# Optimization experiments

Hardware: AMD Instinct MI355X
Metric: run time of the kernel (lower is better)

Reference implementation:

```python
import jax, jax.numpy as jnp
import numpy as np

H = 1024
BATCH, T = 16, 2048

def setup_inputs() -> dict:
    key = jax.random.key(0)
    k1, k2, k3, k4 = jax.random.split(key, 4)
    scale = 1.0 / (H ** 0.5)
    return {
        "u_sequence": jax.random.normal(k1, (BATCH, T, 1), dtype=jnp.float32),
        "A": jax.random.normal(k2, (H, H), dtype=jnp.float32) * scale,
        "B": jax.random.normal(k3, (H, 1), dtype=jnp.float32) * scale,
        "C": jax.random.normal(k4, (1, H), dtype=jnp.float32) * scale,
        "D": jnp.zeros((1,), dtype=jnp.float32),
    }

def reference(u_sequence, A, B, C, D):
    # u_sequence: [Bt, T, 1]
    u = u_sequence[..., 0]            # [Bt, T]
    b_vec = B[:, 0]                   # [H]

    def step(h, u_t):
        # h: [Bt, H], u_t: [Bt]
        h_new = h @ A.T + u_t[:, None] * b_vec[None, :]
        return h_new, h_new

    h0 = jnp.zeros((u.shape[0], H), dtype=u.dtype)
    _, h_stack = jax.lax.scan(step, h0, u.T)   # h_stack: [T, Bt, H]
    h_stack = jnp.swapaxes(h_stack, 0, 1)      # [Bt, T, H]
    y = jnp.einsum("bth,h->bt", h_stack, C[0]) + u * D[0]
    return y[..., None]                         # [Bt, T, 1]
```

## Files before the change

### kernel.cpp

```cpp
#include <hip/hip_runtime.h>

#define HDIM 1024
#define TLEN 2048
#define NBATCH 16

typedef short bf16x8 __attribute__((ext_vector_type(8)));
typedef float floatx4 __attribute__((ext_vector_type(4)));
typedef unsigned short ushort_t;

__device__ __forceinline__ ushort_t f2bf(float x) {
  unsigned u = __float_as_uint(x);
  unsigned r = (u + 0x7FFFu + ((u >> 16) & 1u)) >> 16;
  return (ushort_t)r;
}
__device__ __forceinline__ float bf2f(ushort_t h) {
  return __uint_as_float(((unsigned)h) << 16);
}

typedef __attribute__((address_space(1))) void gvoid_t;
typedef __attribute__((address_space(3))) void lvoid_t;
__device__ __forceinline__ void gload16(const ushort_t* g, ushort_t* l) {
  __builtin_amdgcn_global_load_lds((gvoid_t*)g, (lvoid_t*)l, 16, 0, 0);
}

#define TSTR 71

__global__ __launch_bounds__(256) void prep(const float* __restrict__ A,
    const float* __restrict__ Bv, const float* __restrict__ Cv,
    ushort_t* __restrict__ Ah, ushort_t* __restrict__ Am, ushort_t* __restrict__ Al,
    ushort_t* __restrict__ ATh, ushort_t* __restrict__ ATm, ushort_t* __restrict__ ATl,
    float* __restrict__ Vc, float* __restrict__ U) {
  __shared__ ushort_t Lt[3 * 64 * TSTR];
  const int tid = threadIdx.x;
  if (blockIdx.x >= 256) {
    int i = (blockIdx.x - 256) * 256 + tid;
    if (i < HDIM) Vc[i] = Bv[i];
    else U[i - HDIM] = Cv[i - HDIM];
    return;
  }
  const int row0 = (blockIdx.x >> 4) * 64, col0 = (blockIdx.x & 15) * 64;
  const int r = tid >> 2, q = tid & 3;
  ushort_t hs[16], ms[16], ls[16];
#pragma unroll
  for (int c4 = 0; c4 < 4; ++c4) {
    float4 a = *(const float4*)&A[(row0 + r) * HDIM + col0 + q * 16 + c4 * 4];
    float av[4] = {a.x, a.y, a.z, a.w};
#pragma unroll
    for (int i = 0; i < 4; ++i) {
      float z = av[i];
      ushort_t h = f2bf(z); float r1 = z - bf2f(h);
      ushort_t mq = f2bf(r1); float r2 = r1 - bf2f(mq);
      ushort_t lq = f2bf(r2);
      hs[c4 * 4 + i] = h; ms[c4 * 4 + i] = mq; ls[c4 * 4 + i] = lq;
    }
  }
  size_t go = (size_t)(row0 + r) * HDIM + col0 + q * 16;
  *(uint4*)&Ah[go] = ((uint4*)hs)[0]; *(uint4*)&Ah[go + 8] = ((uint4*)hs)[1];
  *(uint4*)&Am[go] = ((uint4*)ms)[0]; *(uint4*)&Am[go + 8] = ((uint4*)ms)[1];
  *(uint4*)&Al[go] = ((uint4*)ls)[0]; *(uint4*)&Al[go + 8] = ((uint4*)ls)[1];
#pragma unroll
  for (int i = 0; i < 16; ++i) {
    int c = q * 16 + i;
    Lt[0 * 64 * TSTR + r * TSTR + c] = hs[i];
    Lt[1 * 64 * TSTR + r * TSTR + c] = ms[i];
    Lt[2 * 64 * TSTR + r * TSTR + c] = ls[i];
  }
  __syncthreads();
  const int c = tid >> 2, q2 = tid & 3;
  ushort_t* dsts[3] = {ATh, ATm, ATl};
#pragma unroll
  for (int s = 0; s < 3; ++s) {
    ushort_t tmp[16];
#pragma unroll
    for (int rr = 0; rr < 16; ++rr) tmp[rr] = Lt[s * 64 * TSTR + (q2 * 16 + rr) * TSTR + c];
    size_t gt = (size_t)(col0 + c) * HDIM + row0 + q2 * 16;
    *(uint4*)&dsts[s][gt] = ((uint4*)tmp)[0];
    *(uint4*)&dsts[s][gt + 8] = ((uint4*)tmp)[1];
  }
}

template <int MODE, int NC, bool SIX, bool WRITEL>
__global__ __launch_bounds__(256) void sq_mfma(
    const ushort_t* __restrict__ Xh, const ushort_t* __restrict__ Xm,
    const ushort_t* __restrict__ Xl,
    const ushort_t* __restrict__ XTh, const ushort_t* __restrict__ XTm,
    const ushort_t* __restrict__ XTl,
    ushort_t* __restrict__ Zh, ushort_t* __restrict__ Zm, ushort_t* __restrict__ Zl,
    ushort_t* __restrict__ ZTh, ushort_t* __restrict__ ZTm, ushort_t* __restrict__ ZTl,
    const float* __restrict__ Af, const float* __restrict__ Bvf,
    float* __restrict__ VU) {
  constexpr int NARR = SIX ? 6 : 4;
  constexpr int SLAB = 64 * 32;
  constexpr int BUFSTR = NARR * SLAB;
  constexpr int BBASE = (SIX ? 3 : 2) * SLAB;
  constexpr int LDS_ELEMS = 2 * BUFSTR;
  __shared__ __align__(16) ushort_t sm[LDS_ELEMS];
  const int tid = threadIdx.x;

  if (blockIdx.x >= 256) {
    const int tb = blockIdx.x - 256;
    const int wv = tb * 4 + (tid >> 6);
    const int lane = tid & 63;
    if (MODE == 0) {
      float acc = 0.f;
      for (int k = lane; k < HDIM; k += 64) acc += Af[(size_t)wv * HDIM + k] * Bvf[k];
      for (int off = 32; off; off >>= 1) acc += __shfl_down(acc, off);
      if (lane == 0) VU[HDIM + wv] = acc;
    } else {
      const ushort_t* Ph = (MODE == 1) ? Xh : XTh;
      const ushort_t* Pm = (MODE == 1) ? Xm : XTm;
      float acc[NC];
#pragma unroll
      for (int n = 0; n < NC; ++n) acc[n] = 0.f;
      for (int k = lane; k < HDIM; k += 64) {
        float a = bf2f(Ph[(size_t)wv * HDIM + k]) + bf2f(Pm[(size_t)wv * HDIM + k]);
#pragma unroll
        for (int n = 0; n < NC; ++n) acc[n] += a * VU[(size_t)n * HDIM + k];
      }
#pragma unroll
      for (int n = 0; n < NC; ++n) {
        float s = acc[n];
        for (int off = 32; off; off >>= 1) s += __shfl_down(s, off);
        if (lane == 0) VU[(size_t)(NC + n) * HDIM + wv] = s;
      }
    }
    return;
  }

  const int bb = blockIdx.x;
  const int xcd = bb & 7, slot = bb >> 3;
  const int tr = 4 * (xcd >> 1) + (slot >> 3);
  const int tc = 8 * (xcd & 1) + (slot & 7);
  const int row0 = tr * 64, col0 = tc * 64;

  const int w = tid >> 6, l = tid & 63, li = l & 15, quad = l >> 4;
  const int sr = tid >> 2, sq4 = tid & 3;

  floatx4 acc0 = {0.f, 0.f, 0.f, 0.f}, acc1 = acc0, acc2 = acc0, acc3 = acc0;

  const int aoff = (w * 16 + li) * 32 + quad * 8;
  const int b0o = (0 * 16 + li) * 32 + quad * 8;
  const int b1o = (1 * 16 + li) * 32 + quad * 8;
  const int b2o = (2 * 16 + li) * 32 + quad * 8;
  const int b3o = (3 * 16 + li) * 32 + quad * 8;

  const ushort_t* gAh = Xh + (size_t)(row0 + sr) * HDIM + sq4 * 8;
  const ushort_t* gAm = Xm + (size_t)(row0 + sr) * HDIM + sq4 * 8;
  const ushort_t* gAl = Xl + (size_t)(row0 + sr) * HDIM + sq4 * 8;
  const ushort_t* gBh = XTh + (size_t)(col0 + sr) * HDIM + sq4 * 8;
  const ushort_t* gBm = XTm + (size_t)(col0 + sr) * HDIM + sq4 * 8;
  const ushort_t* gBl = XTl + (size_t)(col0 + sr) * HDIM + sq4 * 8;

  ushort_t* lwb = &sm[w * 512];

  {
    ushort_t* lb = lwb;
    gload16(gAh, lb);
    gload16(gAm, lb + SLAB);
    gload16(gBh, lb + BBASE);
    gload16(gBm, lb + BBASE + SLAB);
    if (SIX) {
      gload16(gAl, lb + 2 * SLAB);
      gload16(gBl, lb + BBASE + 2 * SLAB);
    }
  }
  __syncthreads();

  int cur = 0;
  for (int k0 = 0; k0 < HDIM; k0 += 32) {
    if (k0 + 32 < HDIM) {
      ushort_t* lb = lwb + (cur ^ 1) * BUFSTR;
      const int kn = k0 + 32;
      gload16(gAh + kn, lb);
      gload16(gAm + kn, lb + SLAB);
      gload16(gBh + kn, lb + BBASE);
      gload16(gBm + kn, lb + BBASE + SLAB);
      if (SIX) {
        gload16(gAl + kn, lb + 2 * SLAB);
        gload16(gBl + kn, lb + BBASE + 2 * SLAB);
      }
    }
    const int cb = cur * BUFSTR;
    bf16x8 ah = *(const bf16x8*)&sm[cb + aoff];
    bf16x8 am = *(const bf16x8*)&sm[cb + SLAB + aoff];
    bf16x8 al;
    if (SIX) al = *(const bf16x8*)&sm[cb + 2 * SLAB + aoff];
    {
      bf16x8 bh = *(const bf16x8*)&sm[cb + BBASE + b0o];
      bf16x8 bm = *(const bf16x8*)&sm[cb + BBASE + SLAB + b0o];
      acc0 = __builtin_amdgcn_mfma_f32_16x16x32_bf16(ah, bh, acc0, 0, 0, 0);
      acc0 = __builtin_amdgcn_mfma_f32_16x16x32_bf16(ah, bm, acc0, 0, 0, 0);
      acc0 = __builtin_amdgcn_mfma_f32_16x16x32_bf16(am, bh, acc0, 0, 0, 0);
      acc0 = __builtin_amdgcn_mfma_f32_16x16x32_bf16(am, bm, acc0, 0, 0, 0);
      if (SIX) {
        bf16x8 bl = *(const bf16x8*)&sm[cb + BBASE + 2 * SLAB + b0o];
        acc0 = __builtin_amdgcn_mfma_f32_16x16x32_bf16(ah, bl, acc0, 0, 0, 0);
        acc0 = __builtin_amdgcn_mfma_f32_16x16x32_bf16(al, bh, acc0, 0, 0, 0);
      }
    }
    {
      bf16x8 bh = *(const bf16x8*)&sm[cb + BBASE + b1o];
      bf16x8 bm = *(const bf16x8*)&sm[cb + BBASE + SLAB + b1o];
      acc1 = __builtin_amdgcn_mfma_f32_16x16x32_bf16(ah, bh, acc1, 0, 0, 0);
      acc1 = __builtin_amdgcn_mfma_f32_16x16x32_bf16(ah, bm, acc1, 0, 0, 0);
      acc1 = __builtin_amdgcn_mfma_f32_16x16x32_bf16(am, bh, acc1, 0, 0, 0);
      acc1 = __builtin_amdgcn_mfma_f32_16x16x32_bf16(am, bm, acc1, 0, 0, 0);
      if (SIX) {
        bf16x8 bl = *(const bf16x8*)&sm[cb + BBASE + 2 * SLAB + b1o];
        acc1 = __builtin_amdgcn_mfma_f32_16x16x32_bf16(ah, bl, acc1, 0, 0, 0);
        acc1 = __builtin_amdgcn_mfma_f32_16x16x32_bf16(al, bh, acc1, 0, 0, 0);
      }
    }
    {
      bf16x8 bh = *(const bf16x8*)&sm[cb + BBASE + b2o];
      bf16x8 bm = *(const bf16x8*)&sm[cb + BBASE + SLAB + b2o];
      acc2 = __builtin_amdgcn_mfma_f32_16x16x32_bf16(ah, bh, acc2, 0, 0, 0);
      acc2 = __builtin_amdgcn_mfma_f32_16x16x32_bf16(ah, bm, acc2, 0, 0, 0);
      acc2 = __builtin_amdgcn_mfma_f32_16x16x32_bf16(am, bh, acc2, 0, 0, 0);
      acc2 = __builtin_amdgcn_mfma_f32_16x16x32_bf16(am, bm, acc2, 0, 0, 0);
      if (SIX) {
        bf16x8 bl = *(const bf16x8*)&sm[cb + BBASE + 2 * SLAB + b2o];
        acc2 = __builtin_amdgcn_mfma_f32_16x16x32_bf16(ah, bl, acc2, 0, 0, 0);
        acc2 = __builtin_amdgcn_mfma_f32_16x16x32_bf16(al, bh, acc2, 0, 0, 0);
      }
    }
    {
      bf16x8 bh = *(const bf16x8*)&sm[cb + BBASE + b3o];
      bf16x8 bm = *(const bf16x8*)&sm[cb + BBASE + SLAB + b3o];
      acc3 = __builtin_amdgcn_mfma_f32_16x16x32_bf16(ah, bh, acc3, 0, 0, 0);
      acc3 = __builtin_amdgcn_mfma_f32_16x16x32_bf16(ah, bm, acc3, 0, 0, 0);
      acc3 = __builtin_amdgcn_mfma_f32_16x16x32_bf16(am, bh, acc3, 0, 0, 0);
      acc3 = __builtin_amdgcn_mfma_f32_16x16x32_bf16(am, bm, acc3, 0, 0, 0);
      if (SIX) {
        bf16x8 bl = *(const bf16x8*)&sm[cb + BBASE + 2 * SLAB + b3o];
        acc3 = __builtin_amdgcn_mfma_f32_16x16x32_bf16(ah, bl, acc3, 0, 0, 0);
        acc3 = __builtin_amdgcn_mfma_f32_16x16x32_bf16(al, bh, acc3, 0, 0, 0);
      }
    }
    __syncthreads();
    cur ^= 1;
  }

  floatx4 accs[4] = {acc0, acc1, acc2, acc3};
#pragma unroll
  for (int j = 0; j < 4; ++j) {
#pragma unroll
    for (int e = 0; e < 4; ++e) {
      float z = accs[j][e];
      int rl = w * 16 + quad * 4 + e;
      int cl = j * 16 + li;
      size_t go = (size_t)(row0 + rl) * HDIM + col0 + cl;
      ushort_t h = f2bf(z); float r1 = z - bf2f(h);
      ushort_t mq = f2bf(r1);
      Zh[go] = h; Zm[go] = mq;
      sm[0 * 64 * TSTR + rl * TSTR + cl] = h;
      sm[1 * 64 * TSTR + rl * TSTR + cl] = mq;
      if (WRITEL) {
        ushort_t lq = f2bf(r1 - bf2f(mq));
        Zl[go] = lq;
        sm[2 * 64 * TSTR + rl * TSTR + cl] = lq;
      }
    }
  }
  __syncthreads();
  const int c = tid >> 2, q2 = tid & 3;
  ushort_t* dsts[3] = {ZTh, ZTm, ZTl};
  const int npass = WRITEL ? 3 : 2;
#pragma unroll
  for (int s = 0; s < 3; ++s) {
    if (s >= npass) break;
    ushort_t tmp[16];
#pragma unroll
    for (int rr = 0; rr < 16; ++rr) tmp[rr] = sm[s * 64 * TSTR + (q2 * 16 + rr) * TSTR + c];
    size_t gt = (size_t)(col0 + c) * HDIM + row0 + q2 * 16;
    *(uint4*)&dsts[s][gt] = ((uint4*)tmp)[0];
    *(uint4*)&dsts[s][gt + 8] = ((uint4*)tmp)[1];
  }
}

__global__ __launch_bounds__(256) void utail8(const ushort_t* __restrict__ PTh,
                                              const ushort_t* __restrict__ PTm,
                                              float* __restrict__ U, int dstbase) {
  const int wv = blockIdx.x * 4 + (threadIdx.x >> 6);
  const int lane = threadIdx.x & 63;
  float acc[8];
#pragma unroll
  for (int m = 0; m < 8; ++m) acc[m] = 0.f;
  const float* Usrc = U + (size_t)(dstbase - 8) * HDIM;
  for (int k = lane; k < HDIM; k += 64) {
    float a = bf2f(PTh[(size_t)wv * HDIM + k]) + bf2f(PTm[(size_t)wv * HDIM + k]);
#pragma unroll
    for (int m = 0; m < 8; ++m) acc[m] += a * Usrc[(size_t)m * HDIM + k];
  }
#pragma unroll
  for (int m = 0; m < 8; ++m) {
    float s = acc[m];
    for (int off = 32; off; off >>= 1) s += __shfl_down(s, off);
    if (lane == 0) U[(size_t)(dstbase + m) * HDIM + wv] = s;
  }
}

__global__ __launch_bounds__(256) void wavedotK(const float* __restrict__ U,
                                                const float* __restrict__ Vc,
                                                float* __restrict__ Km) {
  int wv = (blockIdx.x * blockDim.x + threadIdx.x) >> 6;
  int lane = threadIdx.x & 63;
  if (wv >= 32 * 64) return;
  int mr = wv >> 6;
  int nc = wv & 63;
  float s = 0.f;
  for (int k = lane; k < HDIM; k += 64) s += U[mr * HDIM + k] * Vc[nc * HDIM + k];
  for (int off = 32; off; off >>= 1) s += __shfl_down(s, off);
  if (lane == 0) Km[wv] = s;
}

__global__ __launch_bounds__(256) void convk2(const float* __restrict__ u,
                                              const float* __restrict__ Km,
                                              const float* __restrict__ Dv,
                                              float* __restrict__ y) {
  __shared__ float ks[256];
  __shared__ float us[512];
  const int tt = threadIdx.x;
  const int t0 = blockIdx.x * 256;
  const int b = blockIdx.y;
  const float* ub = u + (size_t)b * TLEN;
  const int t = t0 + tt;
  float s = Dv[0] * ub[t];
  for (int mc = 0; mc <= t0; mc += 256) {
    __syncthreads();
    ks[tt] = Km[mc + tt];
    int w0 = t0 - mc - 255;
    int g0 = w0 + tt;
    us[tt] = (g0 >= 0) ? ub[g0] : 0.f;
    int g1 = w0 + 256 + tt;
    us[256 + tt] = (g1 < TLEN) ? ub[g1] : 0.f;
    __syncthreads();
    if (mc < t0) {
#pragma unroll 4
      for (int r = 0; r < 256; r += 4) {
        float4 kv = *(const float4*)&ks[r];
        s += kv.x * us[tt - r + 255];
        s += kv.y * us[tt - r + 254];
        s += kv.z * us[tt - r + 253];
        s += kv.w * us[tt - r + 252];
      }
    } else {
      for (int r = 0; r <= tt; ++r) s += ks[r] * us[tt - r + 255];
    }
  }
  y[(size_t)b * TLEN + t] = s;
}

extern "C" void kernel_launch(void* const* d_in, const int* in_sizes, int n_in,
                              void* d_out, int out_size, void* d_ws, size_t ws_size,
                              hipStream_t stream) {
  const float* u  = (const float*)d_in[0];
  const float* A  = (const float*)d_in[1];
  const float* Bv = (const float*)d_in[2];
  const float* Cv = (const float*)d_in[3];
  const float* Dv = (const float*)d_in[4];
  float* out = (float*)d_out;

  char* wsb = (char*)d_ws;
  size_t off = 0;
  ushort_t* S[2][6];
  for (int s = 0; s < 2; ++s)
    for (int a = 0; a < 6; ++a) { S[s][a] = (ushort_t*)(wsb + off); off += (size_t)2 << 20; }
  float* Vc = (float*)(wsb + off); off += 64 * HDIM * 4;
  float* U  = (float*)(wsb + off); off += 32 * HDIM * 4;
  float* Km = (float*)(wsb + off); off += TLEN * 4;

  const dim3 gsq(512);

#define SQ(MODE, NC, SIX, WRL, IN, OUT, VU)                                    \
  sq_mfma<MODE, NC, SIX, WRL><<<gsq, 256, 0, stream>>>(                        \
      S[IN][0], S[IN][1], S[IN][2], S[IN][3], S[IN][4], S[IN][5],              \
      S[OUT][0], S[OUT][1], S[OUT][2], S[OUT][3], S[OUT][4], S[OUT][5],        \
      A, Bv, VU)

  prep<<<dim3(264), 256, 0, stream>>>(A, Bv, Cv,
      S[0][0], S[0][1], S[0][2], S[0][3], S[0][4], S[0][5], Vc, U);

  SQ(0, 1,  true,  true,  0, 1, Vc);
  SQ(1, 2,  true,  true,  1, 0, Vc);
  SQ(1, 4,  true,  true,  0, 1, Vc);
  SQ(1, 8,  true,  false, 1, 0, Vc);
  SQ(1, 16, false, false, 0, 1, Vc);
  SQ(1, 32, false, false, 1, 0, Vc);
  SQ(2, 1,  false, false, 0, 1, U);
  SQ(2, 2,  false, false, 1, 0, U);
  SQ(2, 4,  false, false, 0, 1, U);
#undef SQ

  utail8<<<dim3(256), 256, 0, stream>>>(S[1][3], S[1][4], U, 8);
  utail8<<<dim3(256), 256, 0, stream>>>(S[1][3], S[1][4], U, 16);
  utail8<<<dim3(256), 256, 0, stream>>>(S[1][3], S[1][4], U, 24);

  wavedotK<<<dim3(512), 256, 0, stream>>>(U, Vc, Km);
  convk2<<<dim3(TLEN / 256, NBATCH), 256, 0, stream>>>(u, Km, Dv, out);
}
```

Measured before the change: 315.3 us.

## Use 2x2 warp tiling with swizzled LDS, skip unused row writes, split conv accumulators

The squaring GEMM kernel now gives each wave a 32x32 output subtile (2x2 MFMA tiles) instead of a 16x64 strip, so each loaded A/B fragment is reused twice. It also XOR-swizzles the LDS layout to cut bank conflicts. A new template flag lets the last squaring skip writing row-major outputs that nothing downstream reads, and the convolution kernel uses four independent accumulators to break the FMA dependency chain. The cost is more registers per wave, and the swizzle must stay consistent between the global-to-LDS load addresses and the fragment reads.

```diff
diff --git a/kernel.cpp b/kernel.cpp
--- a/kernel.cpp
+++ b/kernel.cpp
@@ -79,7 +79,7 @@
   }
 }
 
-template <int MODE, int NC, bool SIX, bool WRITEL>
+template <int MODE, int NC, bool SIX, bool WRITEL, bool WROW>
 __global__ __launch_bounds__(256) void sq_mfma(
     const ushort_t* __restrict__ Xh, const ushort_t* __restrict__ Xm,
     const ushort_t* __restrict__ Xl,
@@ -134,15 +134,17 @@
   const int row0 = tr * 64, col0 = tc * 64;
 
   const int w = tid >> 6, l = tid & 63, li = l & 15, quad = l >> 4;
-  const int sr = tid >> 2, sq4 = tid & 3;
-
-  floatx4 acc0 = {0.f, 0.f, 0.f, 0.f}, acc1 = acc0, acc2 = acc0, acc3 = acc0;
-
-  const int aoff = (w * 16 + li) * 32 + quad * 8;
-  const int b0o = (0 * 16 + li) * 32 + quad * 8;
-  const int b1o = (1 * 16 + li) * 32 + quad * 8;
-  const int b2o = (2 * 16 + li) * 32 + quad * 8;
-  const int b3o = (3 * 16 + li) * 32 + quad * 8;
+  const int wr = w >> 1, wc = w & 1;
+  const int sr = tid >> 2;
+  const int sq4 = (tid & 3) ^ ((tid >> 3) & 3);
+
+  floatx4 acc00 = {0.f, 0.f, 0.f, 0.f}, acc01 = acc00, acc10 = acc00, acc11 = acc00;
+
+  const int swz8 = (quad ^ ((li >> 1) & 3)) * 8;
+  const int a0off = (wr * 32 + li) * 32 + swz8;
+  const int a1off = (wr * 32 + 16 + li) * 32 + swz8;
+  const int b0off = (wc * 32 + li) * 32 + swz8;
+  const int b1off = (wc * 32 + 16 + li) * 32 + swz8;
 
   const ushort_t* gAh = Xh + (size_t)(row0 + sr) * HDIM + sq4 * 8;
   const ushort_t* gAm = Xm + (size_t)(row0 + sr) * HDIM + sq4 * 8;
@@ -181,83 +183,76 @@
       }
     }
     const int cb = cur * BUFSTR;
-    bf16x8 ah = *(const bf16x8*)&sm[cb + aoff];
-    bf16x8 am = *(const bf16x8*)&sm[cb + SLAB + aoff];
-    bf16x8 al;
-    if (SIX) al = *(const bf16x8*)&sm[cb + 2 * SLAB + aoff];
-    {
-      bf16x8 bh = *(const bf16x8*)&sm[cb + BBASE + b0o];
-      bf16x8 bm = *(const bf16x8*)&sm[cb + BBASE + SLAB + b0o];
-      acc0 = __builtin_amdgcn_mfma_f32_16x16x32_bf16(ah, bh, acc0, 0, 0, 0);
-      acc0 = __builtin_amdgcn_mfma_f32_16x16x32_bf16(ah, bm, acc0, 0, 0, 0);
-      acc0 = __builtin_amdgcn_mfma_f32_16x16x32_bf16(am, bh, acc0, 0, 0, 0);
-      acc0 = __builtin_amdgcn_mfma_f32_16x16x32_bf16(am, bm, acc0, 0, 0, 0);
-      if (SIX) {
-        bf16x8 bl = *(const bf16x8*)&sm[cb + BBASE + 2 * SLAB + b0o];
-        acc0 = __builtin_amdgcn_mfma_f32_16x16x32_bf16(ah, bl, acc0, 0, 0, 0);
-        acc0 = __builtin_amdgcn_mfma_f32_16x16x32_bf16(al, bh, acc0, 0, 0, 0);
-      }
-    }
-    {
-      bf16x8 bh = *(const bf16x8*)&sm[cb + BBASE + b1o];
-      bf16x8 bm = *(const bf16x8*)&sm[cb + BBASE + SLAB + b1o];
-      acc1 = __builtin_amdgcn_mfma_f32_16x16x32_bf16(ah, bh, acc1, 0, 0, 0);
-      acc1 = __builtin_amdgcn_mfma_f32_16x16x32_bf16(ah, bm, acc1, 0, 0, 0);
-      acc1 = __builtin_amdgcn_mfma_f32_16x16x32_bf16(am, bh, acc1, 0, 0, 0);
-      acc1 = __builtin_amdgcn_mfma_f32_16x16x32_bf16(am, bm, acc1, 0, 0, 0);
-      if (SIX) {
-        bf16x8 bl = *(const bf16x8*)&sm[cb + BBASE + 2 * SLAB + b1o];
-        acc1 = __builtin_amdgcn_mfma_f32_16x16x32_bf16(ah, bl, acc1, 0, 0, 0);
-        acc1 = __builtin_amdgcn_mfma_f32_16x16x32_bf16(al, bh, acc1, 0, 0, 0);
-      }
-    }
-    {
-      bf16x8 bh = *(const bf16x8*)&sm[cb + BBASE + b2o];
-      bf16x8 bm = *(const bf16x8*)&sm[cb + BBASE + SLAB + b2o];
-      acc2 = __builtin_amdgcn_mfma_f32_16x16x32_bf16(ah, bh, acc2, 0, 0, 0);
-      acc2 = __builtin_amdgcn_mfma_f32_16x16x32_bf16(ah, bm, acc2, 0, 0, 0);
-      acc2 = __builtin_amdgcn_mfma_f32_16x16x32_bf16(am, bh, acc2, 0, 0, 0);
-      acc2 = __builtin_amdgcn_mfma_f32_16x16x32_bf16(am, bm, acc2, 0, 0, 0);
-      if (SIX) {
-        bf16x8 bl = *(const bf16x8*)&sm[cb + BBASE + 2 * SLAB + b2o];
-        acc2 = __builtin_amdgcn_mfma_f32_16x16x32_bf16(ah, bl, acc2, 0, 0, 0);
-        acc2 = __builtin_amdgcn_mfma_f32_16x16x32_bf16(al, bh, acc2, 0, 0, 0);
-      }
-    }
-    {
-      bf16x8 bh = *(const bf16x8*)&sm[cb + BBASE + b3o];
-      bf16x8 bm = *(const bf16x8*)&sm[cb + BBASE + SLAB + b3o];
-      acc3 = __builtin_amdgcn_mfma_f32_16x16x32_bf16(ah, bh, acc3, 0, 0, 0);
-      acc3 = __builtin_amdgcn_mfma_f32_16x16x32_bf16(ah, bm, acc3, 0, 0, 0);
-      acc3 = __builtin_amdgcn_mfma_f32_16x16x32_bf16(am, bh, acc3, 0, 0, 0);
-      acc3 = __builtin_amdgcn_mfma_f32_16x16x32_bf16(am, bm, acc3, 0, 0, 0);
-      if (SIX) {
-        bf16x8 bl = *(const bf16x8*)&sm[cb + BBASE + 2 * SLAB + b3o];
-        acc3 = __builtin_amdgcn_mfma_f32_16x16x32_bf16(ah, bl, acc3, 0, 0, 0);
-        acc3 = __builtin_amdgcn_mfma_f32_16x16x32_bf16(al, bh, acc3, 0, 0, 0);
-      }
+    bf16x8 ah0 = *(const bf16x8*)&sm[cb + a0off];
+    bf16x8 am0 = *(const bf16x8*)&sm[cb + SLAB + a0off];
+    bf16x8 ah1 = *(const bf16x8*)&sm[cb + a1off];
+    bf16x8 am1 = *(const bf16x8*)&sm[cb + SLAB + a1off];
+    bf16x8 bh0 = *(const bf16x8*)&sm[cb + BBASE + b0off];
+    bf16x8 bm0 = *(const bf16x8*)&sm[cb + BBASE + SLAB + b0off];
+    bf16x8 bh1 = *(const bf16x8*)&sm[cb + BBASE + b1off];
+    bf16x8 bm1 = *(const bf16x8*)&sm[cb + BBASE + SLAB + b1off];
+    bf16x8 al0, al1, bl0, bl1;
+    if (SIX) {
+      al0 = *(const bf16x8*)&sm[cb + 2 * SLAB + a0off];
+      al1 = *(const bf16x8*)&sm[cb + 2 * SLAB + a1off];
+      bl0 = *(const bf16x8*)&sm[cb + BBASE + 2 * SLAB + b0off];
+      bl1 = *(const bf16x8*)&sm[cb + BBASE + 2 * SLAB + b1off];
+    }
+    acc00 = __builtin_amdgcn_mfma_f32_16x16x32_bf16(ah0, bh0, acc00, 0, 0, 0);
+    acc00 = __builtin_amdgcn_mfma_f32_16x16x32_bf16(ah0, bm0, acc00, 0, 0, 0);
+    acc00 = __builtin_amdgcn_mfma_f32_16x16x32_bf16(am0, bh0, acc00, 0, 0, 0);
+    acc00 = __builtin_amdgcn_mfma_f32_16x16x32_bf16(am0, bm0, acc00, 0, 0, 0);
+    if (SIX) {
+      acc00 = __builtin_amdgcn_mfma_f32_16x16x32_bf16(ah0, bl0, acc00, 0, 0, 0);
+      acc00 = __builtin_amdgcn_mfma_f32_16x16x32_bf16(al0, bh0, acc00, 0, 0, 0);
+    }
+    acc01 = __builtin_amdgcn_mfma_f32_16x16x32_bf16(ah0, bh1, acc01, 0, 0, 0);
+    acc01 = __builtin_amdgcn_mfma_f32_16x16x32_bf16(ah0, bm1, acc01, 0, 0, 0);
+    acc01 = __builtin_amdgcn_mfma_f32_16x16x32_bf16(am0, bh1, acc01, 0, 0, 0);
+    acc01 = __builtin_amdgcn_mfma_f32_16x16x32_bf16(am0, bm1, acc01, 0, 0, 0);
+    if (SIX) {
+      acc01 = __builtin_amdgcn_mfma_f32_16x16x32_bf16(ah0, bl1, acc01, 0, 0, 0);
+      acc01 = __builtin_amdgcn_mfma_f32_16x16x32_bf16(al0, bh1, acc01, 0, 0, 0);
+    }
+    acc10 = __builtin_amdgcn_mfma_f32_16x16x32_bf16(ah1, bh0, acc10, 0, 0, 0);
+    acc10 = __builtin_amdgcn_mfma_f32_16x16x32_bf16(ah1, bm0, acc10, 0, 0, 0);
+    acc10 = __builtin_amdgcn_mfma_f32_16x16x32_bf16(am1, bh0, acc10, 0, 0, 0);
+    acc10 = __builtin_amdgcn_mfma_f32_16x16x32_bf16(am1, bm0, acc10, 0, 0, 0);
+    if (SIX) {
+      acc10 = __builtin_amdgcn_mfma_f32_16x16x32_bf16(ah1, bl0, acc10, 0, 0, 0);
+      acc10 = __builtin_amdgcn_mfma_f32_16x16x32_bf16(al1, bh0, acc10, 0, 0, 0);
+    }
+    acc11 = __builtin_amdgcn_mfma_f32_16x16x32_bf16(ah1, bh1, acc11, 0, 0, 0);
+    acc11 = __builtin_amdgcn_mfma_f32_16x16x32_bf16(ah1, bm1, acc11, 0, 0, 0);
+    acc11 = __builtin_amdgcn_mfma_f32_16x16x32_bf16(am1, bh1, acc11, 0, 0, 0);
+    acc11 = __builtin_amdgcn_mfma_f32_16x16x32_bf16(am1, bm1, acc11, 0, 0, 0);
+    if (SIX) {
+      acc11 = __builtin_amdgcn_mfma_f32_16x16x32_bf16(ah1, bl1, acc11, 0, 0, 0);
+      acc11 = __builtin_amdgcn_mfma_f32_16x16x32_bf16(al1, bh1, acc11, 0, 0, 0);
     }
     __syncthreads();
     cur ^= 1;
   }
 
-  floatx4 accs[4] = {acc0, acc1, acc2, acc3};
-#pragma unroll
-  for (int j = 0; j < 4; ++j) {
+  __syncthreads();
+  floatx4 accs[4] = {acc00, acc01, acc10, acc11};
+#pragma unroll
+  for (int mn = 0; mn < 4; ++mn) {
+    const int m = mn >> 1, n = mn & 1;
 #pragma unroll
     for (int e = 0; e < 4; ++e) {
-      float z = accs[j][e];
-      int rl = w * 16 + quad * 4 + e;
-      int cl = j * 16 + li;
+      float z = accs[mn][e];
+      int rl = wr * 32 + m * 16 + quad * 4 + e;
+      int cl = wc * 32 + n * 16 + li;
       size_t go = (size_t)(row0 + rl) * HDIM + col0 + cl;
       ushort_t h = f2bf(z); float r1 = z - bf2f(h);
       ushort_t mq = f2bf(r1);
-      Zh[go] = h; Zm[go] = mq;
+      if (WROW) { Zh[go] = h; Zm[go] = mq; }
       sm[0 * 64 * TSTR + rl * TSTR + cl] = h;
       sm[1 * 64 * TSTR + rl * TSTR + cl] = mq;
       if (WRITEL) {
         ushort_t lq = f2bf(r1 - bf2f(mq));
-        Zl[go] = lq;
+        if (WROW) Zl[go] = lq;
         sm[2 * 64 * TSTR + rl * TSTR + cl] = lq;
       }
     }
@@ -325,7 +320,7 @@
   const int b = blockIdx.y;
   const float* ub = u + (size_t)b * TLEN;
   const int t = t0 + tt;
-  float s = Dv[0] * ub[t];
+  float s0 = Dv[0] * ub[t], s1 = 0.f, s2 = 0.f, s3 = 0.f;
   for (int mc = 0; mc <= t0; mc += 256) {
     __syncthreads();
     ks[tt] = Km[mc + tt];
@@ -339,16 +334,16 @@
 #pragma unroll 4
       for (int r = 0; r < 256; r += 4) {
         float4 kv = *(const float4*)&ks[r];
-        s += kv.x * us[tt - r + 255];
-        s += kv.y * us[tt - r + 254];
-        s += kv.z * us[tt - r + 253];
-        s += kv.w * us[tt - r + 252];
+        s0 += kv.x * us[tt - r + 255];
+        s1 += kv.y * us[tt - r + 254];
+        s2 += kv.z * us[tt - r + 253];
+        s3 += kv.w * us[tt - r + 252];
       }
     } else {
-      for (int r = 0; r <= tt; ++r) s += ks[r] * us[tt - r + 255];
-    }
-  }
-  y[(size_t)b * TLEN + t] = s;
+      for (int r = 0; r <= tt; ++r) s0 += ks[r] * us[tt - r + 255];
+    }
+  }
+  y[(size_t)b * TLEN + t] = s0 + s1 + s2 + s3;
 }
 
 extern "C" void kernel_launch(void* const* d_in, const int* in_sizes, int n_in,
@@ -372,8 +367,8 @@
 
   const dim3 gsq(512);
 
-#define SQ(MODE, NC, SIX, WRL, IN, OUT, VU)                                    \
-  sq_mfma<MODE, NC, SIX, WRL><<<gsq, 256, 0, stream>>>(                        \
+#define SQ(MODE, NC, SIX, WRL, WROW, IN, OUT, VU)                              \
+  sq_mfma<MODE, NC, SIX, WRL, WROW><<<gsq, 256, 0, stream>>>(                  \
       S[IN][0], S[IN][1], S[IN][2], S[IN][3], S[IN][4], S[IN][5],              \
       S[OUT][0], S[OUT][1], S[OUT][2], S[OUT][3], S[OUT][4], S[OUT][5],        \
       A, Bv, VU)
@@ -381,15 +376,15 @@
   prep<<<dim3(264), 256, 0, stream>>>(A, Bv, Cv,
       S[0][0], S[0][1], S[0][2], S[0][3], S[0][4], S[0][5], Vc, U);
 
-  SQ(0, 1,  true,  true,  0, 1, Vc);
-  SQ(1, 2,  true,  true,  1, 0, Vc);
-  SQ(1, 4,  true,  true,  0, 1, Vc);
-  SQ(1, 8,  true,  false, 1, 0, Vc);
-  SQ(1, 16, false, false, 0, 1, Vc);
-  SQ(1, 32, false, false, 1, 0, Vc);
-  SQ(2, 1,  false, false, 0, 1, U);
-  SQ(2, 2,  false, false, 1, 0, U);
-  SQ(2, 4,  false, false, 0, 1, U);
+  SQ(0, 1,  true,  true,  true,  0, 1, Vc);
+  SQ(1, 2,  true,  true,  true,  1, 0, Vc);
+  SQ(1, 4,  true,  true,  true,  0, 1, Vc);
+  SQ(1, 8,  true,  false, true,  1, 0, Vc);
+  SQ(1, 16, false, false, true,  0, 1, Vc);
+  SQ(1, 32, false, false, true,  1, 0, Vc);
+  SQ(2, 1,  false, false, true,  0, 1, U);
+  SQ(2, 2,  false, false, true,  1, 0, U);
+  SQ(2, 4,  false, false, false, 0, 1, U);
 #undef SQ
 
   utail8<<<dim3(256), 256, 0, stream>>>(S[1][3], S[1][4], U, 8);
```

Measured after the change: 326.4 us. +3.5%, slower.

## Use BK=64 XOR-swizzled LDS tiles for 4-way squaring and skip unused row writes

Applied to the files above, without the earlier changes.

For the non-SIX (hi/mid only) squaring passes, the K-tile doubles from 32 to 64 and the LDS layout gets an XOR swizzle, halving the number of barriers and loop iterations per GEMM. The last squaring pass no longer writes the row-major output arrays, which nothing reads afterwards, saving global stores. The convk2 inner loop splits its accumulator into four independent partial sums to break the serial FMA dependency chain. The larger tile doubles LDS use per block, which may lower occupancy.

```diff
diff --git a/kernel.cpp b/kernel.cpp
--- a/kernel.cpp
+++ b/kernel.cpp
@@ -79,7 +79,7 @@
   }
 }
 
-template <int MODE, int NC, bool SIX, bool WRITEL>
+template <int MODE, int NC, bool SIX, bool WRITEL, bool WROW>
 __global__ __launch_bounds__(256) void sq_mfma(
     const ushort_t* __restrict__ Xh, const ushort_t* __restrict__ Xm,
     const ushort_t* __restrict__ Xl,
@@ -89,9 +89,9 @@
     ushort_t* __restrict__ ZTh, ushort_t* __restrict__ ZTm, ushort_t* __restrict__ ZTl,
     const float* __restrict__ Af, const float* __restrict__ Bvf,
     float* __restrict__ VU) {
-  constexpr int NARR = SIX ? 6 : 4;
-  constexpr int SLAB = 64 * 32;
-  constexpr int BUFSTR = NARR * SLAB;
+  constexpr int BK = SIX ? 32 : 64;
+  constexpr int SLAB = 64 * BK;
+  constexpr int BUFSTR = (SIX ? 6 : 4) * SLAB;
   constexpr int BBASE = (SIX ? 3 : 2) * SLAB;
   constexpr int LDS_ELEMS = 2 * BUFSTR;
   __shared__ __align__(16) ushort_t sm[LDS_ELEMS];
@@ -134,111 +134,177 @@
   const int row0 = tr * 64, col0 = tc * 64;
 
   const int w = tid >> 6, l = tid & 63, li = l & 15, quad = l >> 4;
-  const int sr = tid >> 2, sq4 = tid & 3;
 
   floatx4 acc0 = {0.f, 0.f, 0.f, 0.f}, acc1 = acc0, acc2 = acc0, acc3 = acc0;
 
-  const int aoff = (w * 16 + li) * 32 + quad * 8;
-  const int b0o = (0 * 16 + li) * 32 + quad * 8;
-  const int b1o = (1 * 16 + li) * 32 + quad * 8;
-  const int b2o = (2 * 16 + li) * 32 + quad * 8;
-  const int b3o = (3 * 16 + li) * 32 + quad * 8;
-
-  const ushort_t* gAh = Xh + (size_t)(row0 + sr) * HDIM + sq4 * 8;
-  const ushort_t* gAm = Xm + (size_t)(row0 + sr) * HDIM + sq4 * 8;
-  const ushort_t* gAl = Xl + (size_t)(row0 + sr) * HDIM + sq4 * 8;
-  const ushort_t* gBh = XTh + (size_t)(col0 + sr) * HDIM + sq4 * 8;
-  const ushort_t* gBm = XTm + (size_t)(col0 + sr) * HDIM + sq4 * 8;
-  const ushort_t* gBl = XTl + (size_t)(col0 + sr) * HDIM + sq4 * 8;
-
   ushort_t* lwb = &sm[w * 512];
 
-  {
-    ushort_t* lb = lwb;
-    gload16(gAh, lb);
-    gload16(gAm, lb + SLAB);
-    gload16(gBh, lb + BBASE);
-    gload16(gBm, lb + BBASE + SLAB);
-    if (SIX) {
+  if (SIX) {
+    const int sr = tid >> 2, sq4 = tid & 3;
+    const int aoff = (w * 16 + li) * 32 + quad * 8;
+    const int b0o = (0 * 16 + li) * 32 + quad * 8;
+    const int b1o = (1 * 16 + li) * 32 + quad * 8;
+    const int b2o = (2 * 16 + li) * 32 + quad * 8;
+    const int b3o = (3 * 16 + li) * 32 + quad * 8;
+
+    const ushort_t* gAh = Xh + (size_t)(row0 + sr) * HDIM + sq4 * 8;
+    const ushort_t* gAm = Xm + (size_t)(row0 + sr) * HDIM + sq4 * 8;
+    const ushort_t* gAl = Xl + (size_t)(row0 + sr) * HDIM + sq4 * 8;
+    const ushort_t* gBh = XTh + (size_t)(col0 + sr) * HDIM + sq4 * 8;
+    const ushort_t* gBm = XTm + (size_t)(col0 + sr) * HDIM + sq4 * 8;
+    const ushort_t* gBl = XTl + (size_t)(col0 + sr) * HDIM + sq4 * 8;
+
+    {
+      ushort_t* lb = lwb;
+      gload16(gAh, lb);
+      gload16(gAm, lb + SLAB);
       gload16(gAl, lb + 2 * SLAB);
+      gload16(gBh, lb + BBASE);
+      gload16(gBm, lb + BBASE + SLAB);
       gload16(gBl, lb + BBASE + 2 * SLAB);
     }
-  }
-  __syncthreads();
-
-  int cur = 0;
-  for (int k0 = 0; k0 < HDIM; k0 += 32) {
-    if (k0 + 32 < HDIM) {
-      ushort_t* lb = lwb + (cur ^ 1) * BUFSTR;
-      const int kn = k0 + 32;
-      gload16(gAh + kn, lb);
-      gload16(gAm + kn, lb + SLAB);
-      gload16(gBh + kn, lb + BBASE);
-      gload16(gBm + kn, lb + BBASE + SLAB);
-      if (SIX) {
+    __syncthreads();
+
+    int cur = 0;
+    for (int k0 = 0; k0 < HDIM; k0 += 32) {
+      if (k0 + 32 < HDIM) {
+        ushort_t* lb = lwb + (cur ^ 1) * BUFSTR;
+        const int kn = k0 + 32;
+        gload16(gAh + kn, lb);
+        gload16(gAm + kn, lb + SLAB);
         gload16(gAl + kn, lb + 2 * SLAB);
+        gload16(gBh + kn, lb + BBASE);
+        gload16(gBm + kn, lb + BBASE + SLAB);
         gload16(gBl + kn, lb + BBASE + 2 * SLAB);
       }
-    }
-    const int cb = cur * BUFSTR;
-    bf16x8 ah = *(const bf16x8*)&sm[cb + aoff];
-    bf16x8 am = *(const bf16x8*)&sm[cb + SLAB + aoff];
-    bf16x8 al;
-    if (SIX) al = *(const bf16x8*)&sm[cb + 2 * SLAB + aoff];
-    {
-      bf16x8 bh = *(const bf16x8*)&sm[cb + BBASE + b0o];
-      bf16x8 bm = *(const bf16x8*)&sm[cb + BBASE + SLAB + b0o];
-      acc0 = __builtin_amdgcn_mfma_f32_16x16x32_bf16(ah, bh, acc0, 0, 0, 0);
-      acc0 = __builtin_amdgcn_mfma_f32_16x16x32_bf16(ah, bm, acc0, 0, 0, 0);
-      acc0 = __builtin_amdgcn_mfma_f32_16x16x32_bf16(am, bh, acc0, 0, 0, 0);
-      acc0 = __builtin_amdgcn_mfma_f32_16x16x32_bf16(am, bm, acc0, 0, 0, 0);
-      if (SIX) {
+      const int cb = cur * BUFSTR;
+      bf16x8 ah = *(const bf16x8*)&sm[cb + aoff];
+      bf16x8 am = *(const bf16x8*)&sm[cb + SLAB + aoff];
+      bf16x8 al = *(const bf16x8*)&sm[cb + 2 * SLAB + aoff];
+      {
+        bf16x8 bh = *(const bf16x8*)&sm[cb + BBASE + b0o];
+        bf16x8 bm = *(const bf16x8*)&sm[cb + BBASE + SLAB + b0o];
         bf16x8 bl = *(const bf16x8*)&sm[cb + BBASE + 2 * SLAB + b0o];
+        acc0 = __builtin_amdgcn_mfma_f32_16x16x32_bf16(ah, bh, acc0, 0, 0, 0);
+        acc0 = __builtin_amdgcn_mfma_f32_16x16x32_bf16(ah, bm, acc0, 0, 0, 0);
+        acc0 = __builtin_amdgcn_mfma_f32_16x16x32_bf16(am, bh, acc0, 0, 0, 0);
+        acc0 = __builtin_amdgcn_mfma_f32_16x16x32_bf16(am, bm, acc0, 0, 0, 0);
         acc0 = __builtin_amdgcn_mfma_f32_16x16x32_bf16(ah, bl, acc0, 0, 0, 0);
         acc0 = __builtin_amdgcn_mfma_f32_16x16x32_bf16(al, bh, acc0, 0, 0, 0);
       }
-    }
-    {
-      bf16x8 bh = *(const bf16x8*)&sm[cb + BBASE + b1o];
-      bf16x8 bm = *(const bf16x8*)&sm[cb + BBASE + SLAB + b1o];
-      acc1 = __builtin_amdgcn_mfma_f32_16x16x32_bf16(ah, bh, acc1, 0, 0, 0);
-      acc1 = __builtin_amdgcn_mfma_f32_16x16x32_bf16(ah, bm, acc1, 0, 0, 0);
-      acc1 = __builtin_amdgcn_mfma_f32_16x16x32_bf16(am, bh, acc1, 0, 0, 0);
-      acc1 = __builtin_amdgcn_mfma_f32_16x16x32_bf16(am, bm, acc1, 0, 0, 0);
-      if (SIX) {
+      {
+        bf16x8 bh = *(const bf16x8*)&sm[cb + BBASE + b1o];
+        bf16x8 bm = *(const bf16x8*)&sm[cb + BBASE + SLAB + b1o];
         bf16x8 bl = *(const bf16x8*)&sm[cb + BBASE + 2 * SLAB + b1o];
+        acc1 = __builtin_amdgcn_mfma_f32_16x16x32_bf16(ah, bh, acc1, 0, 0, 0);
+        acc1 = __builtin_amdgcn_mfma_f32_16x16x32_bf16(ah, bm, acc1, 0, 0, 0);
+        acc1 = __builtin_amdgcn_mfma_f32_16x16x32_bf16(am, bh, acc1, 0, 0, 0);
+        acc1 = __builtin_amdgcn_mfma_f32_16x16x32_bf16(am, bm, acc1, 0, 0, 0);
         acc1 = __builtin_amdgcn_mfma_f32_16x16x32_bf16(ah, bl, acc1, 0, 0, 0);
         acc1 = __builtin_amdgcn_mfma_f32_16x16x32_bf16(al, bh, acc1, 0, 0, 0);
       }
-    }
-    {
-      bf16x8 bh = *(const bf16x8*)&sm[cb + BBASE + b2o];
-      bf16x8 bm = *(const bf16x8*)&sm[cb + BBASE + SLAB + b2o];
-      acc2 = __builtin_amdgcn_mfma_f32_16x16x32_bf16(ah, bh, acc2, 0, 0, 0);
-      acc2 = __builtin_amdgcn_mfma_f32_16x16x32_bf16(ah, bm, acc2, 0, 0, 0);
-      acc2 = __builtin_amdgcn_mfma_f32_16x16x32_bf16(am, bh, acc2, 0, 0, 0);
-      acc2 = __builtin_amdgcn_mfma_f32_16x16x32_bf16(am, bm, acc2, 0, 0, 0);
-      if (SIX) {
+      {
+        bf16x8 bh = *(const bf16x8*)&sm[cb + BBASE + b2o];
+        bf16x8 bm = *(const bf16x8*)&sm[cb + BBASE + SLAB + b2o];
         bf16x8 bl = *(const bf16x8*)&sm[cb + BBASE + 2 * SLAB + b2o];
+        acc2 = __builtin_amdgcn_mfma_f32_16x16x32_bf16(ah, bh, acc2, 0, 0, 0);
+        acc2 = __builtin_amdgcn_mfma_f32_16x16x32_bf16(ah, bm, acc2, 0, 0, 0);
+        acc2 = __builtin_amdgcn_mfma_f32_16x16x32_bf16(am, bh, acc2, 0, 0, 0);
+        acc2 = __builtin_amdgcn_mfma_f32_16x16x32_bf16(am, bm, acc2, 0, 0, 0);
         acc2 = __builtin_amdgcn_mfma_f32_16x16x32_bf16(ah, bl, acc2, 0, 0, 0);
         acc2 = __builtin_amdgcn_mfma_f32_16x16x32_bf16(al, bh, acc2, 0, 0, 0);
       }
-    }
-    {
-      bf16x8 bh = *(const bf16x8*)&sm[cb + BBASE + b3o];
-      bf16x8 bm = *(const bf16x8*)&sm[cb + BBASE + SLAB + b3o];
-      acc3 = __builtin_amdgcn_mfma_f32_16x16x32_bf16(ah, bh, acc3, 0, 0, 0);
-      acc3 = __builtin_amdgcn_mfma_f32_16x16x32_bf16(ah, bm, acc3, 0, 0, 0);
-      acc3 = __builtin_amdgcn_mfma_f32_16x16x32_bf16(am, bh, acc3, 0, 0, 0);
-      acc3 = __builtin_amdgcn_mfma_f32_16x16x32_bf16(am, bm, acc3, 0, 0, 0);
-      if (SIX) {
+      {
+        bf16x8 bh = *(const bf16x8*)&sm[cb + BBASE + b3o];
+        bf16x8 bm = *(const bf16x8*)&sm[cb + BBASE + SLAB + b3o];
         bf16x8 bl = *(const bf16x8*)&sm[cb + BBASE + 2 * SLAB + b3o];
+        acc3 = __builtin_amdgcn_mfma_f32_16x16x32_bf16(ah, bh, acc3, 0, 0, 0);
+        acc3 = __builtin_amdgcn_mfma_f32_16x16x32_bf16(ah, bm, acc3, 0, 0, 0);
+        acc3 = __builtin_amdgcn_mfma_f32_16x16x32_bf16(am, bh, acc3, 0, 0, 0);
+        acc3 = __builtin_amdgcn_mfma_f32_16x16x32_bf16(am, bm, acc3, 0, 0, 0);
         acc3 = __builtin_amdgcn_mfma_f32_16x16x32_bf16(ah, bl, acc3, 0, 0, 0);
         acc3 = __builtin_amdgcn_mfma_f32_16x16x32_bf16(al, bh, acc3, 0, 0, 0);
       }
+      __syncthreads();
+      cur ^= 1;
+    }
+  } else {
+    const int sr8 = tid >> 3;
+    const int kq8 = (tid & 7) ^ (sr8 & 7);
+    const ushort_t* gAh = Xh + (size_t)(row0 + sr8) * HDIM + kq8 * 8;
+    const ushort_t* gAm = Xm + (size_t)(row0 + sr8) * HDIM + kq8 * 8;
+    const ushort_t* gBh = XTh + (size_t)(col0 + sr8) * HDIM + kq8 * 8;
+    const ushort_t* gBm = XTm + (size_t)(col0 + sr8) * HDIM + kq8 * 8;
+    const size_t p1 = (size_t)32 * HDIM;
+
+    const int j0 = (quad ^ (li & 7)) * 8;
+    const int aoff = (w * 16 + li) * 64 + j0;
+    const int b0o = (0 * 16 + li) * 64 + j0;
+    const int b1o = (1 * 16 + li) * 64 + j0;
+    const int b2o = (2 * 16 + li) * 64 + j0;
+    const int b3o = (3 * 16 + li) * 64 + j0;
+
+    {
+      ushort_t* lb = lwb;
+      gload16(gAh, lb);              gload16(gAh + p1, lb + 2048);
+      gload16(gAm, lb + SLAB);       gload16(gAm + p1, lb + SLAB + 2048);
+      gload16(gBh, lb + BBASE);      gload16(gBh + p1, lb + BBASE + 2048);
+      gload16(gBm, lb + BBASE + SLAB); gload16(gBm + p1, lb + BBASE + SLAB + 2048);
     }
     __syncthreads();
-    cur ^= 1;
+
+    int cur = 0;
+    for (int k0 = 0; k0 < HDIM; k0 += 64) {
+      if (k0 + 64 < HDIM) {
+        ushort_t* lb = lwb + (cur ^ 1) * BUFSTR;
+        const int kn = k0 + 64;
+        gload16(gAh + kn, lb);              gload16(gAh + p1 + kn, lb + 2048);
+        gload16(gAm + kn, lb + SLAB);       gload16(gAm + p1 + kn, lb + SLAB + 2048);
+        gload16(gBh + kn, lb + BBASE);      gload16(gBh + p1 + kn, lb + BBASE + 2048);
+        gload16(gBm + kn, lb + BBASE + SLAB); gload16(gBm + p1 + kn, lb + BBASE + SLAB + 2048);
+      }
+      const int cb = cur * BUFSTR;
+#pragma unroll
+      for (int cc = 0; cc < 2; ++cc) {
+        const int cx = cc * 32;
+        bf16x8 ah = *(const bf16x8*)&sm[cb + (aoff ^ cx)];
+        bf16x8 am = *(const bf16x8*)&sm[cb + SLAB + (aoff ^ cx)];
+        {
+          bf16x8 bh = *(const bf16x8*)&sm[cb + BBASE + (b0o ^ cx)];
+          bf16x8 bm = *(const bf16x8*)&sm[cb + BBASE + SLAB + (b0o ^ cx)];
+          acc0 = __builtin_amdgcn_mfma_f32_16x16x32_bf16(ah, bh, acc0, 0, 0, 0);
+          acc0 = __builtin_amdgcn_mfma_f32_16x16x32_bf16(ah, bm, acc0, 0, 0, 0);
+          acc0 = __builtin_amdgcn_mfma_f32_16x16x32_bf16(am, bh, acc0, 0, 0, 0);
+          acc0 = __builtin_amdgcn_mfma_f32_16x16x32_bf16(am, bm, acc0, 0, 0, 0);
+        }
+        {
+          bf16x8 bh = *(const bf16x8*)&sm[cb + BBASE + (b1o ^ cx)];
+          bf16x8 bm = *(const bf16x8*)&sm[cb + BBASE + SLAB + (b1o ^ cx)];
+          acc1 = __builtin_amdgcn_mfma_f32_16x16x32_bf16(ah, bh, acc1, 0, 0, 0);
+          acc1 = __builtin_amdgcn_mfma_f32_16x16x32_bf16(ah, bm, acc1, 0, 0, 0);
+          acc1 = __builtin_amdgcn_mfma_f32_16x16x32_bf16(am, bh, acc1, 0, 0, 0);
+          acc1 = __builtin_amdgcn_mfma_f32_16x16x32_bf16(am, bm, acc1, 0, 0, 0);
+        }
+        {
+          bf16x8 bh = *(const bf16x8*)&sm[cb + BBASE + (b2o ^ cx)];
+          bf16x8 bm = *(const bf16x8*)&sm[cb + BBASE + SLAB + (b2o ^ cx)];
+          acc2 = __builtin_amdgcn_mfma_f32_16x16x32_bf16(ah, bh, acc2, 0, 0, 0);
+          acc2 = __builtin_amdgcn_mfma_f32_16x16x32_bf16(ah, bm, acc2, 0, 0, 0);
+          acc2 = __builtin_amdgcn_mfma_f32_16x16x32_bf16(am, bh, acc2, 0, 0, 0);
+          acc2 = __builtin_amdgcn_mfma_f32_16x16x32_bf16(am, bm, acc2, 0, 0, 0);
+        }
+        {
+          bf16x8 bh = *(const bf16x8*)&sm[cb + BBASE + (b3o ^ cx)];
+          bf16x8 bm = *(const bf16x8*)&sm[cb + BBASE + SLAB + (b3o ^ cx)];
+          acc3 = __builtin_amdgcn_mfma_f32_16x16x32_bf16(ah, bh, acc3, 0, 0, 0);
+          acc3 = __builtin_amdgcn_mfma_f32_16x16x32_bf16(ah, bm, acc3, 0, 0, 0);
+          acc3 = __builtin_amdgcn_mfma_f32_16x16x32_bf16(am, bh, acc3, 0, 0, 0);
+          acc3 = __builtin_amdgcn_mfma_f32_16x16x32_bf16(am, bm, acc3, 0, 0, 0);
+        }
+      }
+      __syncthreads();
+      cur ^= 1;
+    }
   }
 
   floatx4 accs[4] = {acc0, acc1, acc2, acc3};
@@ -252,12 +318,12 @@
       size_t go = (size_t)(row0 + rl) * HDIM + col0 + cl;
       ushort_t h = f2bf(z); float r1 = z - bf2f(h);
       ushort_t mq = f2bf(r1);
-      Zh[go] = h; Zm[go] = mq;
+      if (WROW) { Zh[go] = h; Zm[go] = mq; }
       sm[0 * 64 * TSTR + rl * TSTR + cl] = h;
       sm[1 * 64 * TSTR + rl * TSTR + cl] = mq;
       if (WRITEL) {
         ushort_t lq = f2bf(r1 - bf2f(mq));
-        Zl[go] = lq;
+        if (WROW) Zl[go] = lq;
         sm[2 * 64 * TSTR + rl * TSTR + cl] = lq;
       }
     }
@@ -325,7 +391,7 @@
   const int b = blockIdx.y;
   const float* ub = u + (size_t)b * TLEN;
   const int t = t0 + tt;
-  float s = Dv[0] * ub[t];
+  float s0 = Dv[0] * ub[t], s1 = 0.f, s2 = 0.f, s3 = 0.f;
   for (int mc = 0; mc <= t0; mc += 256) {
     __syncthreads();
     ks[tt] = Km[mc + tt];
@@ -339,16 +405,16 @@
 #pragma unroll 4
       for (int r = 0; r < 256; r += 4) {
         float4 kv = *(const float4*)&ks[r];
-        s += kv.x * us[tt - r + 255];
-        s += kv.y * us[tt - r + 254];
-        s += kv.z * us[tt - r + 253];
-        s += kv.w * us[tt - r + 252];
+        s0 += kv.x * us[tt - r + 255];
+        s1 += kv.y * us[tt - r + 254];
+        s2 += kv.z * us[tt - r + 253];
+        s3 += kv.w * us[tt - r + 252];
       }
     } else {
-      for (int r = 0; r <= tt; ++r) s += ks[r] * us[tt - r + 255];
-    }
-  }
-  y[(size_t)b * TLEN + t] = s;
+      for (int r = 0; r <= tt; ++r) s0 += ks[r] * us[tt - r + 255];
+    }
+  }
+  y[(size_t)b * TLEN + t] = s0 + s1 + s2 + s3;
 }
 
 extern "C" void kernel_launch(void* const* d_in, const int* in_sizes, int n_in,
@@ -372,8 +438,8 @@
 
   const dim3 gsq(512);
 
-#define SQ(MODE, NC, SIX, WRL, IN, OUT, VU)                                    \
-  sq_mfma<MODE, NC, SIX, WRL><<<gsq, 256, 0, stream>>>(                        \
+#define SQ(MODE, NC, SIX, WRL, WROW, IN, OUT, VU)                              \
+  sq_mfma<MODE, NC, SIX, WRL, WROW><<<gsq, 256, 0, stream>>>(                  \
       S[IN][0], S[IN][1], S[IN][2], S[IN][3], S[IN][4], S[IN][5],              \
       S[OUT][0], S[OUT][1], S[OUT][2], S[OUT][3], S[OUT][4], S[OUT][5],        \
       A, Bv, VU)
@@ -381,15 +447,15 @@
   prep<<<dim3(264), 256, 0, stream>>>(A, Bv, Cv,
       S[0][0], S[0][1], S[0][2], S[0][3], S[0][4], S[0][5], Vc, U);
 
-  SQ(0, 1,  true,  true,  0, 1, Vc);
-  SQ(1, 2,  true,  true,  1, 0, Vc);
-  SQ(1, 4,  true,  true,  0, 1, Vc);
-  SQ(1, 8,  true,  false, 1, 0, Vc);
-  SQ(1, 16, false, false, 0, 1, Vc);
-  SQ(1, 32, false, false, 1, 0, Vc);
-  SQ(2, 1,  false, false, 0, 1, U);
-  SQ(2, 2,  false, false, 1, 0, U);
-  SQ(2, 4,  false, false, 0, 1, U);
+  SQ(0, 1,  true,  true,  true,  0, 1, Vc);
+  SQ(1, 2,  true,  true,  true,  1, 0, Vc);
+  SQ(1, 4,  true,  true,  true,  0, 1, Vc);
+  SQ(1, 8,  true,  false, true,  1, 0, Vc);
+  SQ(1, 16, false, false, true,  0, 1, Vc);
+  SQ(1, 32, false, false, true,  1, 0, Vc);
+  SQ(2, 1,  false, false, true,  0, 1, U);
+  SQ(2, 2,  false, false, true,  1, 0, U);
+  SQ(2, 4,  false, false, false, 0, 1, U);
 #undef SQ
 
   utail8<<<dim3(256), 256, 0, stream>>>(S[1][3], S[1][4], U, 8);
```

Result: slower. 351.6 us, median of 2 (+11.5%).

## Triple-buffer MFMA squaring pipeline with vmcnt waits, skip unused row writes

Applied to the files above, without the earlier changes.

Changes the repeated-squaring MFMA kernel from double to triple buffering. Tiles are prefetched two steps ahead, and the full __syncthreads is replaced by explicit vmcnt waits plus a raw s_barrier. A WROW template flag skips the row-major global stores on the last squaring, whose output is only read in transposed form. The convolution inner loop is split across four independent accumulators to break the serial FMA dependency chain. Costs are 50% more LDS per block, which may lower occupancy, and a different float summation order.

```diff
diff --git a/kernel.cpp b/kernel.cpp
--- a/kernel.cpp
+++ b/kernel.cpp
@@ -21,6 +21,19 @@
 typedef __attribute__((address_space(3))) void lvoid_t;
 __device__ __forceinline__ void gload16(const ushort_t* g, ushort_t* l) {
   __builtin_amdgcn_global_load_lds((gvoid_t*)g, (lvoid_t*)l, 16, 0, 0);
+}
+
+template <int N>
+__device__ __forceinline__ void vmwait() {
+  if constexpr (N == 0) asm volatile("s_waitcnt vmcnt(0)" ::: "memory");
+  else if constexpr (N == 4) asm volatile("s_waitcnt vmcnt(4)" ::: "memory");
+  else asm volatile("s_waitcnt vmcnt(6)" ::: "memory");
+}
+__device__ __forceinline__ void phase_barrier() {
+  __builtin_amdgcn_sched_barrier(0);
+  __builtin_amdgcn_s_barrier();
+  __builtin_amdgcn_sched_barrier(0);
+  asm volatile("" ::: "memory");
 }
 
 #define TSTR 71
@@ -79,7 +92,7 @@
   }
 }
 
-template <int MODE, int NC, bool SIX, bool WRITEL>
+template <int MODE, int NC, bool SIX, bool WRITEL, bool WROW>
 __global__ __launch_bounds__(256) void sq_mfma(
     const ushort_t* __restrict__ Xh, const ushort_t* __restrict__ Xm,
     const ushort_t* __restrict__ Xl,
@@ -93,7 +106,7 @@
   constexpr int SLAB = 64 * 32;
   constexpr int BUFSTR = NARR * SLAB;
   constexpr int BBASE = (SIX ? 3 : 2) * SLAB;
-  constexpr int LDS_ELEMS = 2 * BUFSTR;
+  constexpr int LDS_ELEMS = 3 * BUFSTR;
   __shared__ __align__(16) ushort_t sm[LDS_ELEMS];
   const int tid = threadIdx.x;
 
@@ -153,33 +166,26 @@
 
   ushort_t* lwb = &sm[w * 512];
 
-  {
-    ushort_t* lb = lwb;
-    gload16(gAh, lb);
-    gload16(gAm, lb + SLAB);
-    gload16(gBh, lb + BBASE);
-    gload16(gBm, lb + BBASE + SLAB);
-    if (SIX) {
-      gload16(gAl, lb + 2 * SLAB);
-      gload16(gBl, lb + BBASE + 2 * SLAB);
-    }
-  }
-  __syncthreads();
-
-  int cur = 0;
+#define STAGE(BUF, K)                                                          \
+  {                                                                            \
+    ushort_t* lb = lwb + (BUF) * BUFSTR;                                       \
+    const int kk = (K);                                                        \
+    gload16(gAh + kk, lb);                                                     \
+    gload16(gAm + kk, lb + SLAB);                                              \
+    if (SIX) gload16(gAl + kk, lb + 2 * SLAB);                                 \
+    gload16(gBh + kk, lb + BBASE);                                             \
+    gload16(gBm + kk, lb + BBASE + SLAB);                                      \
+    if (SIX) gload16(gBl + kk, lb + BBASE + 2 * SLAB);                         \
+  }
+
+  STAGE(0, 0)
+  STAGE(1, 32)
+  vmwait<NARR>();
+  phase_barrier();
+
+  int cur = 0, nx2 = 2;
   for (int k0 = 0; k0 < HDIM; k0 += 32) {
-    if (k0 + 32 < HDIM) {
-      ushort_t* lb = lwb + (cur ^ 1) * BUFSTR;
-      const int kn = k0 + 32;
-      gload16(gAh + kn, lb);
-      gload16(gAm + kn, lb + SLAB);
-      gload16(gBh + kn, lb + BBASE);
-      gload16(gBm + kn, lb + BBASE + SLAB);
-      if (SIX) {
-        gload16(gAl + kn, lb + 2 * SLAB);
-        gload16(gBl + kn, lb + BBASE + 2 * SLAB);
-      }
-    }
+    if (k0 + 64 < HDIM) STAGE(nx2, k0 + 64)
     const int cb = cur * BUFSTR;
     bf16x8 ah = *(const bf16x8*)&sm[cb + aoff];
     bf16x8 am = *(const bf16x8*)&sm[cb + SLAB + aoff];
@@ -237,9 +243,13 @@
         acc3 = __builtin_amdgcn_mfma_f32_16x16x32_bf16(al, bh, acc3, 0, 0, 0);
       }
     }
-    __syncthreads();
-    cur ^= 1;
-  }
+    asm volatile("" ::: "memory");
+    if (k0 + 64 < HDIM) vmwait<NARR>(); else vmwait<0>();
+    phase_barrier();
+    cur = (cur == 2) ? 0 : cur + 1;
+    nx2 = (nx2 == 2) ? 0 : nx2 + 1;
+  }
+#undef STAGE
 
   floatx4 accs[4] = {acc0, acc1, acc2, acc3};
 #pragma unroll
@@ -252,12 +262,12 @@
       size_t go = (size_t)(row0 + rl) * HDIM + col0 + cl;
       ushort_t h = f2bf(z); float r1 = z - bf2f(h);
       ushort_t mq = f2bf(r1);
-      Zh[go] = h; Zm[go] = mq;
+      if (WROW) { Zh[go] = h; Zm[go] = mq; }
       sm[0 * 64 * TSTR + rl * TSTR + cl] = h;
       sm[1 * 64 * TSTR + rl * TSTR + cl] = mq;
       if (WRITEL) {
         ushort_t lq = f2bf(r1 - bf2f(mq));
-        Zl[go] = lq;
+        if (WROW) Zl[go] = lq;
         sm[2 * 64 * TSTR + rl * TSTR + cl] = lq;
       }
     }
@@ -325,7 +335,7 @@
   const int b = blockIdx.y;
   const float* ub = u + (size_t)b * TLEN;
   const int t = t0 + tt;
-  float s = Dv[0] * ub[t];
+  float s0 = Dv[0] * ub[t], s1 = 0.f, s2 = 0.f, s3 = 0.f;
   for (int mc = 0; mc <= t0; mc += 256) {
     __syncthreads();
     ks[tt] = Km[mc + tt];
@@ -339,16 +349,16 @@
 #pragma unroll 4
       for (int r = 0; r < 256; r += 4) {
         float4 kv = *(const float4*)&ks[r];
-        s += kv.x * us[tt - r + 255];
-        s += kv.y * us[tt - r + 254];
-        s += kv.z * us[tt - r + 253];
-        s += kv.w * us[tt - r + 252];
+        s0 += kv.x * us[tt - r + 255];
+        s1 += kv.y * us[tt - r + 254];
+        s2 += kv.z * us[tt - r + 253];
+        s3 += kv.w * us[tt - r + 252];
       }
     } else {
-      for (int r = 0; r <= tt; ++r) s += ks[r] * us[tt - r + 255];
-    }
-  }
-  y[(size_t)b * TLEN + t] = s;
+      for (int r = 0; r <= tt; ++r) s0 += ks[r] * us[tt - r + 255];
+    }
+  }
+  y[(size_t)b * TLEN + t] = s0 + s1 + s2 + s3;
 }
 
 extern "C" void kernel_launch(void* const* d_in, const int* in_sizes, int n_in,
@@ -372,8 +382,8 @@
 
   const dim3 gsq(512);
 
-#define SQ(MODE, NC, SIX, WRL, IN, OUT, VU)                                    \
-  sq_mfma<MODE, NC, SIX, WRL><<<gsq, 256, 0, stream>>>(                        \
+#define SQ(MODE, NC, SIX, WRL, WROW, IN, OUT, VU)                              \
+  sq_mfma<MODE, NC, SIX, WRL, WROW><<<gsq, 256, 0, stream>>>(                  \
       S[IN][0], S[IN][1], S[IN][2], S[IN][3], S[IN][4], S[IN][5],              \
       S[OUT][0], S[OUT][1], S[OUT][2], S[OUT][3], S[OUT][4], S[OUT][5],        \
       A, Bv, VU)
@@ -381,15 +391,15 @@
   prep<<<dim3(264), 256, 0, stream>>>(A, Bv, Cv,
       S[0][0], S[0][1], S[0][2], S[0][3], S[0][4], S[0][5], Vc, U);
 
-  SQ(0, 1,  true,  true,  0, 1, Vc);
-  SQ(1, 2,  true,  true,  1, 0, Vc);
-  SQ(1, 4,  true,  true,  0, 1, Vc);
-  SQ(1, 8,  true,  false, 1, 0, Vc);
-  SQ(1, 16, false, false, 0, 1, Vc);
-  SQ(1, 32, false, false, 1, 0, Vc);
-  SQ(2, 1,  false, false, 0, 1, U);
-  SQ(2, 2,  false, false, 1, 0, U);
-  SQ(2, 4,  false, false, 0, 1, U);
+  SQ(0, 1,  true,  true,  true,  0, 1, Vc);
+  SQ(1, 2,  true,  true,  true,  1, 0, Vc);
+  SQ(1, 4,  true,  true,  true,  0, 1, Vc);
+  SQ(1, 8,  true,  false, true,  1, 0, Vc);
+  SQ(1, 16, false, false, true,  0, 1, Vc);
+  SQ(1, 32, false, false, true,  1, 0, Vc);
+  SQ(2, 1,  false, false, true,  0, 1, U);
+  SQ(2, 2,  false, false, true,  1, 0, U);
+  SQ(2, 4,  false, false, false, 0, 1, U);
 #undef SQ
 
   utail8<<<dim3(256), 256, 0, stream>>>(S[1][3], S[1][4], U, 8);
```

After: 301.9 us. 4.2% less time.
